# Performance work log

Hardware: AMD Instinct MI355X
Metric: run time of the kernel (lower is better)

## Reference

```python
import jax, jax.numpy as jnp
import numpy as np

V, E, H = 50000, 300, 256  # vocab, word dim, per-direction hidden (nfeat_sent=2H=512)
B, T = 256, 64
NEG = -1e9


def _lstm_scan(x, mask, w_ih, w_hh, b):
    """x: [T,B,E], mask: [T,B,1] float. Masked steps keep (h,c) unchanged.
    Gate order matches torch.nn.LSTM: i, f, g, o."""
    Bsz = x.shape[1]
    Hd = w_hh.shape[1]
    init = (jnp.zeros((Bsz, Hd), x.dtype), jnp.zeros((Bsz, Hd), x.dtype))

    def step(carry, inp):
        h, c = carry
        xt, mt = inp
        z = xt @ w_ih.T + h @ w_hh.T + b  # [B,4H]
        i, f, g, o = jnp.split(z, 4, axis=-1)
        i = jax.nn.sigmoid(i); f = jax.nn.sigmoid(f)
        g = jnp.tanh(g); o = jax.nn.sigmoid(o)
        c_new = f * c + i * g
        h_new = o * jnp.tanh(c_new)
        c = mt * c_new + (1.0 - mt) * c
        h = mt * h_new + (1.0 - mt) * h
        return (h, c), h

    _, hs = jax.lax.scan(step, init, (x, mask))
    return hs  # [T,B,H]


def setup_inputs() -> dict:
    key = jax.random.key(0)
    ks = jax.random.split(key, 9)
    token_ids = jax.random.randint(ks[0], (B, T), 0, V, dtype=jnp.int32)
    lengths = jax.random.randint(ks[1], (B,), 1, T + 1, dtype=jnp.int32)
    emb = jax.random.normal(ks[2], (V, E), jnp.float32) * 0.1
    s = 0.05
    w_ih_f = jax.random.normal(ks[3], (4 * H, E), jnp.float32) * s
    w_hh_f = jax.random.normal(ks[4], (4 * H, H), jnp.float32) * s
    b_f = jax.random.normal(ks[5], (4 * H,), jnp.float32) * s  # b_ih + b_hh fused
    w_ih_b = jax.random.normal(ks[6], (4 * H, E), jnp.float32) * s
    w_hh_b = jax.random.normal(ks[7], (4 * H, H), jnp.float32) * s
    b_b = jax.random.normal(ks[8], (4 * H,), jnp.float32) * s
    return {"token_ids": token_ids, "lengths": lengths, "emb": emb,
            "w_ih_f": w_ih_f, "w_hh_f": w_hh_f, "b_f": b_f,
            "w_ih_b": w_ih_b, "w_hh_b": w_hh_b, "b_b": b_b}


def reference(token_ids, lengths, emb, w_ih_f, w_hh_f, b_f, w_ih_b, w_hh_b, b_b):
    # Batched equivalent of the per-sentence loop: embed -> biLSTM -> max over time.
    x = emb[token_ids]                              # [B,T,E]
    x = jnp.swapaxes(x, 0, 1)                       # [T,B,E] (time-major)
    valid = (jnp.arange(T)[:, None] < lengths[None, :])  # [T,B]
    mask = valid.astype(x.dtype)[:, :, None]        # [T,B,1]

    h_fwd = _lstm_scan(x, mask, w_ih_f, w_hh_f, b_f)  # [T,B,H]
    # Backward direction: reverse time; masked (pad) steps leave state at zero,
    # so each sentence's backward pass starts exactly at its last real token.
    h_bwd = _lstm_scan(x[::-1], mask[::-1], w_ih_b, w_hh_b, b_b)[::-1]

    out = jnp.concatenate([h_fwd, h_bwd], axis=-1)  # [T,B,2H]
    out = jnp.where(valid[:, :, None], out, NEG)
    return jnp.max(out, axis=0)                     # [B, 2H] == [B, nfeat_sent]
```

## Files before the change

### kernel.cpp

```cpp
#include <hip/hip_runtime.h>
#include <hip/hip_bf16.h>
#include <math.h>

#define VV 50000
#define EE 300
#define HD 256
#define BB 256
#define TT 64
#define NEGV -1e9f

#define OFF_HF   0
#define OFF_CTR  524288
#define OFF_B2   526336
#define OFF_WHHF 528384
#define OFF_WIHF 1052672
#define WS_FULL_BYTES (1380352ULL * 4ULL)
#define FB_H 0
#define FB_C 262144

typedef __attribute__((ext_vector_type(8))) short bf16x8;
typedef __attribute__((ext_vector_type(4))) float f32x4;

__device__ __forceinline__ float sigf(float x) {
  return 1.f / (1.f + __expf(-x));
}
__device__ __forceinline__ float tanhfast(float x) {
  return 1.f - 2.f / (__expf(2.f * x) + 1.f);
}
__device__ __forceinline__ unsigned short f2bf(float f) {
  union { float f; unsigned u; } x;
  x.f = f;
  unsigned r = x.u + 0x7fffu + ((x.u >> 16) & 1u);
  return (unsigned short)(r >> 16);
}

__global__ __launch_bounds__(256) void prep_all(
    const float* __restrict__ whf, const float* __restrict__ whb,
    const float* __restrict__ wif, const float* __restrict__ wib,
    const float* __restrict__ bf, const float* __restrict__ bb,
    float* __restrict__ ws) {
  int idx = blockIdx.x * 256 + threadIdx.x;
  if (idx < 131072) ws[OFF_HF + idx] = 0.f;
  if (idx < 2048) {
    ((unsigned int*)(ws + OFF_CTR))[idx] = 0u;
    int dir = idx >> 10, jg = idx & 1023, j = jg >> 2, g = jg & 3;
    ws[OFF_B2 + idx] = (dir ? bb : bf)[g * HD + j];
  }
  if (idx < 65536) {
    int lane = idx & 63, kt = (idx >> 6) & 7, ngrp = (idx >> 9) & 63,
        dir = idx >> 15;
    int n = ngrp * 16 + (lane & 15);
    int j = n >> 2, g = n & 3;
    int k0 = kt * 32 + (lane >> 4) * 8;
    const float* W = dir ? whb : whf;
    const float* src = W + (size_t)((g << 8) + j) * HD + k0;
    union { unsigned short u[8]; uint4 q; } hp, lp;
#pragma unroll
    for (int e = 0; e < 8; ++e) {
      float v = src[e];
      unsigned short hh = f2bf(v);
      union { unsigned u; float f; } hf;
      hf.u = (unsigned)hh << 16;
      hp.u[e] = hh;
      lp.u[e] = f2bf(v - hf.f);
    }
    unsigned short* dst = (unsigned short*)(ws + OFF_WHHF) + (size_t)idx * 16;
    *(uint4*)dst = hp.q;
    *(uint4*)(dst + 8) = lp.q;
  }
  if (idx < 81920) {
    int lane = idx & 63;
    int f = idx >> 6;
    int kt = f % 10;
    int ngrp = (f / 10) & 63;
    int dir = f / 640;
    int n = ngrp * 16 + (lane & 15);
    int j = n >> 2, g = n & 3;
    int k0 = kt * 32 + (lane >> 4) * 8;
    const float* W = dir ? wib : wif;
    union { unsigned short u[8]; uint4 q; } p;
#pragma unroll
    for (int e = 0; e < 8; ++e) {
      int k = k0 + e;
      p.u[e] = (k < EE) ? f2bf(W[(size_t)((g << 8) + j) * EE + k])
                        : (unsigned short)0;
    }
    *(uint4*)((unsigned short*)(ws + OFF_WIHF) + (size_t)idx * 8) = p.q;
  }
}

__global__ __launch_bounds__(256) void init_kernel(float* __restrict__ ws,
                                                   float* __restrict__ out) {
  int idx = blockIdx.x * 256 + threadIdx.x;
  if (idx < 393216) ws[idx] = 0.f;
  if (idx < BB * 2 * HD) out[idx] = NEGV;
}

__global__ __launch_bounds__(512) void lstm_persist(
    const int* __restrict__ tok, const int* __restrict__ lens,
    const float* __restrict__ emb, float* __restrict__ ws,
    float* __restrict__ out) {
  const int bg = blockIdx.x;
  const int slice = blockIdx.y;
  const int dir = blockIdx.z;
  const int tid = threadIdx.x;
  const int lane = tid & 63;
  const int wv = tid >> 6;

  __shared__ __align__(16) unsigned short hfr[2][512][8];
  __shared__ __align__(16) unsigned short ebuf[2][5120];

  bf16x8 whi[8], wlo[8], wih[10];
  const int ngrp = slice * 8 + wv;
  {
    const unsigned short* p = (const unsigned short*)(ws + OFF_WHHF) +
                              (size_t)(((dir * 64 + ngrp) * 8) * 64 + lane) * 16;
#pragma unroll
    for (int kt = 0; kt < 8; ++kt) {
      whi[kt] = *(const bf16x8*)(p + kt * 1024);
      wlo[kt] = *(const bf16x8*)(p + kt * 1024 + 8);
    }
    const unsigned short* q = (const unsigned short*)(ws + OFF_WIHF) +
                              (size_t)(((dir * 64 + ngrp) * 10) * 64 + lane) * 8;
#pragma unroll
    for (int kt = 0; kt < 10; ++kt) wih[kt] = *(const bf16x8*)(q + kt * 512);
  }

  const int rg = tid >> 5;
  const int k8 = tid & 31;
  const int stage_row = bg * 16 + rg;
  const int strow = stage_row * TT;
  const int o2 = 32 + (k8 & 7);
  const bool has2 = (k8 < 8);
  const int slot1 = (k8 >> 2) * 64 + rg * 4 + (k8 & 3);
  const int slot2 = ((o2 >> 2) * 64) + rg * 4 + (o2 & 3);

  const int q = lane & 3;
  const int base = lane & 12;
  const int r = (lane >> 4) * 4 + q;
  const int gate_row = bg * 16 + r;
  const int len = lens[gate_row];
  const int jloc = ngrp * 4 + (base >> 2);
  const float4 bias4 =
      *(const float4*)(ws + OFF_B2 + dir * 1024 + ngrp * 16 + base);
  const int slot_j = (jloc >> 5) * 64 + r * 4 + ((jloc >> 3) & 3);
  const int e_j = jloc & 7;

  const int ld_slot = (lane & 15) * 4 + (lane >> 4);

  unsigned int* ctr =
      (unsigned int*)(ws + OFF_CTR) + (size_t)(dir * 16 + bg) * 32;
  unsigned short* hfg = (unsigned short*)(ws + OFF_HF);

  float c = 0.f, omax = NEGV, h_prev = 0.f;

  {
    const int t0 = dir ? (TT - 1) : 0;
    const float* er = emb + (size_t)tok[strow + t0] * EE;
    float4 a0 = *(const float4*)(er + k8 * 8);
    float4 a1 = *(const float4*)(er + k8 * 8 + 4);
    union { unsigned short u[8]; uint4 q; } p;
    p.u[0] = f2bf(a0.x); p.u[1] = f2bf(a0.y); p.u[2] = f2bf(a0.z);
    p.u[3] = f2bf(a0.w); p.u[4] = f2bf(a1.x); p.u[5] = f2bf(a1.y);
    p.u[6] = f2bf(a1.z); p.u[7] = f2bf(a1.w);
    *(uint4*)&ebuf[0][slot1 * 8] = p.q;
    if (has2) {
      float4 b0 = make_float4(0.f, 0.f, 0.f, 0.f);
      float4 b1 = make_float4(0.f, 0.f, 0.f, 0.f);
      if (o2 <= 37) b0 = *(const float4*)(er + o2 * 8);
      if (o2 < 37) b1 = *(const float4*)(er + o2 * 8 + 4);
      union { unsigned short u[8]; uint4 q; } p2;
      p2.u[0] = f2bf(b0.x); p2.u[1] = f2bf(b0.y); p2.u[2] = f2bf(b0.z);
      p2.u[3] = f2bf(b0.w); p2.u[4] = f2bf(b1.x); p2.u[5] = f2bf(b1.y);
      p2.u[6] = f2bf(b1.z); p2.u[7] = f2bf(b1.w);
      *(uint4*)&ebuf[0][slot2 * 8] = p2.q;
    }
  }

  for (int s = 0; s < TT; ++s) {
    const int t = dir ? (TT - 1 - s) : s;
    const bool nstage = (s < TT - 1);
    const unsigned long long* hsrc = (const unsigned long long*)(
        hfg + (size_t)(((s & 1) * 2 + dir) * 16 + bg) * 8192);
    unsigned long long hu0 = __hip_atomic_load(hsrc + tid * 4 + 0,
                                               __ATOMIC_RELAXED,
                                               __HIP_MEMORY_SCOPE_AGENT);
    unsigned long long hu1 = __hip_atomic_load(hsrc + tid * 4 + 1,
                                               __ATOMIC_RELAXED,
                                               __HIP_MEMORY_SCOPE_AGENT);
    unsigned long long hu2 = __hip_atomic_load(hsrc + tid * 4 + 2,
                                               __ATOMIC_RELAXED,
                                               __HIP_MEMORY_SCOPE_AGENT);
    unsigned long long hu3 = __hip_atomic_load(hsrc + tid * 4 + 3,
                                               __ATOMIC_RELAXED,
                                               __HIP_MEMORY_SCOPE_AGENT);
    float4 pe0, pe1, qe0, qe1;
    if (nstage) {
      const int tn = dir ? (TT - 2 - s) : (s + 1);
      const float* er = emb + (size_t)tok[strow + tn] * EE;
      pe0 = *(const float4*)(er + k8 * 8);
      pe1 = *(const float4*)(er + k8 * 8 + 4);
      qe0 = make_float4(0.f, 0.f, 0.f, 0.f);
      qe1 = make_float4(0.f, 0.f, 0.f, 0.f);
      if (has2) {
        if (o2 <= 37) qe0 = *(const float4*)(er + o2 * 8);
        if (o2 < 37) qe1 = *(const float4*)(er + o2 * 8 + 4);
      }
    }
    {
      unsigned long long* hdst_l = (unsigned long long*)hfr;
      hdst_l[tid * 4 + 0] = hu0;
      hdst_l[tid * 4 + 1] = hu1;
      hdst_l[tid * 4 + 2] = hu2;
      hdst_l[tid * 4 + 3] = hu3;
    }
    __syncthreads();
    f32x4 acc[4];
#pragma unroll
    for (int i = 0; i < 4; ++i) {
      acc[i][0] = 0.f; acc[i][1] = 0.f; acc[i][2] = 0.f; acc[i][3] = 0.f;
    }
    const unsigned short* eb = ebuf[s & 1];
#pragma unroll
    for (int kt = 0; kt < 10; ++kt) {
      bf16x8 ax = *(const bf16x8*)(eb + (kt * 64 + ld_slot) * 8);
      acc[kt & 3] =
          __builtin_amdgcn_mfma_f32_16x16x32_bf16(ax, wih[kt], acc[kt & 3], 0, 0, 0);
    }
#pragma unroll
    for (int kt = 0; kt < 8; ++kt) {
      bf16x8 ahi = *(const bf16x8*)&hfr[0][kt * 64 + ld_slot][0];
      bf16x8 alo = *(const bf16x8*)&hfr[1][kt * 64 + ld_slot][0];
      f32x4 a = acc[kt & 3];
      a = __builtin_amdgcn_mfma_f32_16x16x32_bf16(ahi, whi[kt], a, 0, 0, 0);
      a = __builtin_amdgcn_mfma_f32_16x16x32_bf16(alo, whi[kt], a, 0, 0, 0);
      a = __builtin_amdgcn_mfma_f32_16x16x32_bf16(ahi, wlo[kt], a, 0, 0, 0);
      acc[kt & 3] = a;
    }
    f32x4 zf = (acc[0] + acc[1]) + (acc[2] + acc[3]);
    float v0 = zf[0], v1 = zf[1], v2 = zf[2], v3 = zf[3];
    {
      float s0 = __shfl_xor(v1, 1), s1 = __shfl_xor(v0, 1);
      float s2 = __shfl_xor(v3, 1), s3 = __shfl_xor(v2, 1);
      const bool qb = (q & 1) != 0;
      float a0 = qb ? s0 : v0;
      float a1 = qb ? v1 : s1;
      float a2 = qb ? s2 : v2;
      float a3 = qb ? v3 : s3;
      float t0 = __shfl_xor(a2, 2), t1 = __shfl_xor(a3, 2);
      float t2 = __shfl_xor(a0, 2), t3 = __shfl_xor(a1, 2);
      const bool q2 = (q & 2) != 0;
      v0 = q2 ? t0 : a0;
      v1 = q2 ? t1 : a1;
      v2 = q2 ? a2 : t2;
      v3 = q2 ? a3 : t3;
    }
    float h_out = h_prev;
    if (t < len) {
      float ig = sigf(v0 + bias4.x);
      float fg = sigf(v1 + bias4.y);
      float gg = tanhfast(v2 + bias4.z);
      float og = sigf(v3 + bias4.w);
      c = fg * c + ig * gg;
      float hn = og * tanhfast(c);
      h_out = hn;
      omax = fmaxf(omax, hn);
    }
    h_prev = h_out;
    if (nstage) {
      unsigned short hi = f2bf(h_out);
      union { unsigned u; float f; } hf;
      hf.u = (unsigned)hi << 16;
      unsigned short lo = f2bf(h_out - hf.f);
      unsigned short* hdst =
          hfg + (size_t)((((s + 1) & 1) * 2 + dir) * 16 + bg) * 8192;
      __hip_atomic_store(hdst + slot_j * 8 + e_j, hi, __ATOMIC_RELAXED,
                         __HIP_MEMORY_SCOPE_AGENT);
      __hip_atomic_store(hdst + 4096 + slot_j * 8 + e_j, lo, __ATOMIC_RELAXED,
                         __HIP_MEMORY_SCOPE_AGENT);
      unsigned short* ebn = ebuf[(s + 1) & 1];
      {
        union { unsigned short u[8]; uint4 q; } p;
        p.u[0] = f2bf(pe0.x); p.u[1] = f2bf(pe0.y); p.u[2] = f2bf(pe0.z);
        p.u[3] = f2bf(pe0.w); p.u[4] = f2bf(pe1.x); p.u[5] = f2bf(pe1.y);
        p.u[6] = f2bf(pe1.z); p.u[7] = f2bf(pe1.w);
        *(uint4*)&ebn[slot1 * 8] = p.q;
        if (has2) {
          union { unsigned short u[8]; uint4 q; } p2;
          p2.u[0] = f2bf(qe0.x); p2.u[1] = f2bf(qe0.y); p2.u[2] = f2bf(qe0.z);
          p2.u[3] = f2bf(qe0.w); p2.u[4] = f2bf(qe1.x); p2.u[5] = f2bf(qe1.y);
          p2.u[6] = f2bf(qe1.z); p2.u[7] = f2bf(qe1.w);
          *(uint4*)&ebn[slot2 * 8] = p2.q;
        }
      }
      asm volatile("s_waitcnt vmcnt(0)" ::: "memory");
      __syncthreads();
      if (tid == 0) {
        __hip_atomic_fetch_add(ctr, 1u, __ATOMIC_RELAXED,
                               __HIP_MEMORY_SCOPE_AGENT);
      }
      if (tid < 64) {
        const unsigned int target = 8u * (unsigned)(s + 1);
        while (__hip_atomic_load(ctr, __ATOMIC_RELAXED,
                                 __HIP_MEMORY_SCOPE_AGENT) < target) {
        }
      }
      __syncthreads();
      asm volatile("" ::: "memory");
    }
  }
  out[(size_t)gate_row * (2 * HD) + dir * HD + jloc] = omax;
}

__global__ __launch_bounds__(256) void step_fused(
    const int* __restrict__ tok, const int* __restrict__ lens,
    const float* __restrict__ emb,
    const float* __restrict__ wih_f, const float* __restrict__ whh_f,
    const float* __restrict__ bias_f,
    const float* __restrict__ wih_b, const float* __restrict__ whh_b,
    const float* __restrict__ bias_b,
    float* __restrict__ ws, float* __restrict__ out, int s) {
  const int tid = threadIdx.x;
  const int jt = blockIdx.x, bt = blockIdx.y, dir = blockIdx.z;
  const int j0 = jt * 32, b0g = bt * 16;
  const int t = (dir == 0) ? s : (TT - 1 - s);
  const float* Wih = dir ? wih_b : wih_f;
  const float* Whh = dir ? whh_b : whh_f;
  const float* bias = dir ? bias_b : bias_f;
  const float* hcur = ws + FB_H + (size_t)((s & 1) * 2 + dir) * BB * HD;
  float* hnxt = ws + FB_H + (size_t)(((s + 1) & 1) * 2 + dir) * BB * HD;
  float* cbuf = ws + FB_C + (size_t)dir * BB * HD;

  __shared__ float a_sm[16][64];
  __shared__ float w_sm[64][132];
  __shared__ float z_sm[16][132];

  const int cg = tid & 31, bgr = tid >> 5;
  float acc[2][4] = {{0.f, 0.f, 0.f, 0.f}, {0.f, 0.f, 0.f, 0.f}};

  for (int phase = 0; phase < 2; ++phase) {
    const float* W = phase ? Whh : Wih;
    const int K = phase ? HD : EE;
    for (int k0 = 0; k0 < K; k0 += 64) {
      const int klen = (K - k0) < 64 ? (K - k0) : 64;
      {
        int bl = tid >> 4, kk4 = tid & 15;
        if (kk4 * 4 < klen) {
          const float* src;
          if (phase == 0) {
            int tk = tok[(b0g + bl) * TT + t];
            src = emb + (size_t)tk * EE + k0 + kk4 * 4;
          } else {
            src = hcur + (size_t)(b0g + bl) * HD + k0 + kk4 * 4;
          }
          *(float4*)&a_sm[bl][kk4 * 4] = *(const float4*)src;
        }
      }
      for (int i = 0; i < 8; ++i) {
        int e = i * 256 + tid;
        int col = e >> 4, kk4 = e & 15;
        if (kk4 * 4 < klen) {
          int gcol = ((col >> 5) * HD) + j0 + (col & 31);
          float4 v = *(const float4*)(W + (size_t)gcol * K + k0 + kk4 * 4);
          w_sm[kk4 * 4 + 0][col] = v.x;
          w_sm[kk4 * 4 + 1][col] = v.y;
          w_sm[kk4 * 4 + 2][col] = v.z;
          w_sm[kk4 * 4 + 3][col] = v.w;
        }
      }
      __syncthreads();
      for (int k = 0; k < klen; ++k) {
        float a0 = a_sm[bgr * 2 + 0][k];
        float a1 = a_sm[bgr * 2 + 1][k];
        float4 w = *(const float4*)&w_sm[k][cg * 4];
        acc[0][0] += a0 * w.x; acc[0][1] += a0 * w.y;
        acc[0][2] += a0 * w.z; acc[0][3] += a0 * w.w;
        acc[1][0] += a1 * w.x; acc[1][1] += a1 * w.y;
        acc[1][2] += a1 * w.z; acc[1][3] += a1 * w.w;
      }
      __syncthreads();
    }
  }
  *(float4*)&z_sm[bgr * 2 + 0][cg * 4] =
      make_float4(acc[0][0], acc[0][1], acc[0][2], acc[0][3]);
  *(float4*)&z_sm[bgr * 2 + 1][cg * 4] =
      make_float4(acc[1][0], acc[1][1], acc[1][2], acc[1][3]);
  __syncthreads();
  for (int pi = 0; pi < 2; ++pi) {
    int p = pi * 256 + tid;
    int bl = p >> 5, jl = p & 31;
    int bglob = b0g + bl, jglob = j0 + jl;
    bool valid = t < lens[bglob];
    float h_old = hcur[(size_t)bglob * HD + jglob];
    float h_out = h_old;
    if (valid) {
      float zi = z_sm[bl][0 + jl] + bias[0 * HD + jglob];
      float zf = z_sm[bl][32 + jl] + bias[1 * HD + jglob];
      float zg = z_sm[bl][64 + jl] + bias[2 * HD + jglob];
      float zo = z_sm[bl][96 + jl] + bias[3 * HD + jglob];
      float ig = sigf(zi), fg = sigf(zf), gg = tanhf(zg), og = sigf(zo);
      float c_old = cbuf[(size_t)bglob * HD + jglob];
      float c_new = fg * c_old + ig * gg;
      float h_new = og * tanhf(c_new);
      cbuf[(size_t)bglob * HD + jglob] = c_new;
      h_out = h_new;
      float* op = out + (size_t)bglob * (2 * HD) + dir * HD + jglob;
      *op = fmaxf(*op, h_new);
    }
    hnxt[(size_t)bglob * HD + jglob] = h_out;
  }
}

extern "C" void kernel_launch(void* const* d_in, const int* in_sizes, int n_in,
                              void* d_out, int out_size, void* d_ws,
                              size_t ws_size, hipStream_t stream) {
  const int* tok = (const int*)d_in[0];
  const int* lens = (const int*)d_in[1];
  const float* emb = (const float*)d_in[2];
  const float* wih_f = (const float*)d_in[3];
  const float* whh_f = (const float*)d_in[4];
  const float* b_f = (const float*)d_in[5];
  const float* wih_b = (const float*)d_in[6];
  const float* whh_b = (const float*)d_in[7];
  const float* b_b = (const float*)d_in[8];
  float* out = (float*)d_out;
  float* ws = (float*)d_ws;

  const bool full = ws_size >= WS_FULL_BYTES;
  if (full) {
    hipLaunchKernelGGL(prep_all, dim3(512), dim3(256), 0, stream, whh_f,
                       whh_b, wih_f, wih_b, b_f, b_b, ws);
    hipLaunchKernelGGL(lstm_persist, dim3(16, 8, 2), dim3(512), 0, stream,
                       tok, lens, emb, ws, out);
  } else {
    hipLaunchKernelGGL(init_kernel, dim3(1536), dim3(256), 0, stream, ws, out);
    for (int s = 0; s < TT; ++s) {
      hipLaunchKernelGGL(step_fused, dim3(8, 16, 2), dim3(256), 0, stream, tok,
                         lens, emb, wih_f, whh_f, b_f, wih_b, whh_b, b_b, ws,
                         out, s);
    }
  }
}
```

Baseline: 229.1 us.

## Coalesce recurrent h exchange through LDS staging and swizzle LDS slots

Each block now stages its new hidden-state values (bf16 hi/lo pairs) in a shared-memory tile and has 128 threads write them to global memory as packed 64-bit atomic stores. Before, every thread issued two scattered 16-bit atomic stores. The LDS slot layout for embeddings and h fragments is XOR-swizzled to reduce bank conflicts on the MFMA operand reads, and the global h load pattern is changed to match. This adds an extra __syncthreads and an LDS round trip per time step on the critical recurrent path, in exchange for far fewer global store transactions before the cross-block barrier.

```diff
diff --git a/kernel.cpp b/kernel.cpp
--- a/kernel.cpp
+++ b/kernel.cpp
@@ -109,6 +109,7 @@
 
   __shared__ __align__(16) unsigned short hfr[2][512][8];
   __shared__ __align__(16) unsigned short ebuf[2][5120];
+  __shared__ unsigned int hx[16][36];
 
   bf16x8 whi[8], wlo[8], wih[10];
   const int ngrp = slice * 8 + wv;
@@ -132,8 +133,9 @@
   const int strow = stage_row * TT;
   const int o2 = 32 + (k8 & 7);
   const bool has2 = (k8 < 8);
-  const int slot1 = (k8 >> 2) * 64 + rg * 4 + (k8 & 3);
-  const int slot2 = ((o2 >> 2) * 64) + rg * 4 + (o2 & 3);
+  const int swz_r = (rg >> 1) & 3;
+  const int slot1 = (k8 >> 2) * 64 + rg * 4 + ((k8 & 3) ^ swz_r);
+  const int slot2 = (o2 >> 2) * 64 + rg * 4 + ((o2 & 3) ^ swz_r);
 
   const int q = lane & 3;
   const int base = lane & 12;
@@ -141,12 +143,12 @@
   const int gate_row = bg * 16 + r;
   const int len = lens[gate_row];
   const int jloc = ngrp * 4 + (base >> 2);
+  const int jl32 = wv * 4 + (base >> 2);
   const float4 bias4 =
       *(const float4*)(ws + OFF_B2 + dir * 1024 + ngrp * 16 + base);
-  const int slot_j = (jloc >> 5) * 64 + r * 4 + ((jloc >> 3) & 3);
-  const int e_j = jloc & 7;
-
-  const int ld_slot = (lane & 15) * 4 + (lane >> 4);
+
+  const int ld_r = lane & 15, ld_oct = lane >> 4;
+  const int ld_slot = ld_r * 4 + (ld_oct ^ ((ld_r >> 1) & 3));
 
   unsigned int* ctr =
       (unsigned int*)(ws + OFF_CTR) + (size_t)(dir * 16 + bg) * 32;
@@ -182,18 +184,18 @@
     const bool nstage = (s < TT - 1);
     const unsigned long long* hsrc = (const unsigned long long*)(
         hfg + (size_t)(((s & 1) * 2 + dir) * 16 + bg) * 8192);
-    unsigned long long hu0 = __hip_atomic_load(hsrc + tid * 4 + 0,
-                                               __ATOMIC_RELAXED,
-                                               __HIP_MEMORY_SCOPE_AGENT);
-    unsigned long long hu1 = __hip_atomic_load(hsrc + tid * 4 + 1,
-                                               __ATOMIC_RELAXED,
-                                               __HIP_MEMORY_SCOPE_AGENT);
-    unsigned long long hu2 = __hip_atomic_load(hsrc + tid * 4 + 2,
-                                               __ATOMIC_RELAXED,
-                                               __HIP_MEMORY_SCOPE_AGENT);
-    unsigned long long hu3 = __hip_atomic_load(hsrc + tid * 4 + 3,
-                                               __ATOMIC_RELAXED,
-                                               __HIP_MEMORY_SCOPE_AGENT);
+    unsigned long long a0 = __hip_atomic_load(hsrc + 2 * tid + 0,
+                                              __ATOMIC_RELAXED,
+                                              __HIP_MEMORY_SCOPE_AGENT);
+    unsigned long long a1 = __hip_atomic_load(hsrc + 2 * tid + 1,
+                                              __ATOMIC_RELAXED,
+                                              __HIP_MEMORY_SCOPE_AGENT);
+    unsigned long long b0 = __hip_atomic_load(hsrc + 1024 + 2 * tid + 0,
+                                              __ATOMIC_RELAXED,
+                                              __HIP_MEMORY_SCOPE_AGENT);
+    unsigned long long b1 = __hip_atomic_load(hsrc + 1024 + 2 * tid + 1,
+                                              __ATOMIC_RELAXED,
+                                              __HIP_MEMORY_SCOPE_AGENT);
     float4 pe0, pe1, qe0, qe1;
     if (nstage) {
       const int tn = dir ? (TT - 2 - s) : (s + 1);
@@ -208,11 +210,14 @@
       }
     }
     {
-      unsigned long long* hdst_l = (unsigned long long*)hfr;
-      hdst_l[tid * 4 + 0] = hu0;
-      hdst_l[tid * 4 + 1] = hu1;
-      hdst_l[tid * 4 + 2] = hu2;
-      hdst_l[tid * 4 + 3] = hu3;
+      unsigned long long* l0 =
+          (unsigned long long*)((char*)&hfr[0][0][0] + tid * 16);
+      l0[0] = a0;
+      l0[1] = a1;
+      unsigned long long* l1 =
+          (unsigned long long*)((char*)&hfr[0][0][0] + 8192 + tid * 16);
+      l1[0] = b0;
+      l1[1] = b1;
     }
     __syncthreads();
     f32x4 acc[4];
@@ -243,17 +248,17 @@
       float s0 = __shfl_xor(v1, 1), s1 = __shfl_xor(v0, 1);
       float s2 = __shfl_xor(v3, 1), s3 = __shfl_xor(v2, 1);
       const bool qb = (q & 1) != 0;
-      float a0 = qb ? s0 : v0;
-      float a1 = qb ? v1 : s1;
-      float a2 = qb ? s2 : v2;
-      float a3 = qb ? v3 : s3;
-      float t0 = __shfl_xor(a2, 2), t1 = __shfl_xor(a3, 2);
-      float t2 = __shfl_xor(a0, 2), t3 = __shfl_xor(a1, 2);
+      float t0a = qb ? s0 : v0;
+      float t1a = qb ? v1 : s1;
+      float t2a = qb ? s2 : v2;
+      float t3a = qb ? v3 : s3;
+      float u0 = __shfl_xor(t2a, 2), u1 = __shfl_xor(t3a, 2);
+      float u2 = __shfl_xor(t0a, 2), u3 = __shfl_xor(t1a, 2);
       const bool q2 = (q & 2) != 0;
-      v0 = q2 ? t0 : a0;
-      v1 = q2 ? t1 : a1;
-      v2 = q2 ? a2 : t2;
-      v3 = q2 ? a3 : t3;
+      v0 = q2 ? u0 : t0a;
+      v1 = q2 ? u1 : t1a;
+      v2 = q2 ? t2a : u2;
+      v3 = q2 ? t3a : u3;
     }
     float h_out = h_prev;
     if (t < len) {
@@ -268,16 +273,13 @@
     }
     h_prev = h_out;
     if (nstage) {
-      unsigned short hi = f2bf(h_out);
-      union { unsigned u; float f; } hf;
-      hf.u = (unsigned)hi << 16;
-      unsigned short lo = f2bf(h_out - hf.f);
-      unsigned short* hdst =
-          hfg + (size_t)((((s + 1) & 1) * 2 + dir) * 16 + bg) * 8192;
-      __hip_atomic_store(hdst + slot_j * 8 + e_j, hi, __ATOMIC_RELAXED,
-                         __HIP_MEMORY_SCOPE_AGENT);
-      __hip_atomic_store(hdst + 4096 + slot_j * 8 + e_j, lo, __ATOMIC_RELAXED,
-                         __HIP_MEMORY_SCOPE_AGENT);
+      {
+        unsigned short hi = f2bf(h_out);
+        union { unsigned u; float f; } hf;
+        hf.u = (unsigned)hi << 16;
+        unsigned short lo = f2bf(h_out - hf.f);
+        hx[r][jl32] = ((unsigned)hi << 16) | (unsigned)lo;
+      }
       unsigned short* ebn = ebuf[(s + 1) & 1];
       {
         union { unsigned short u[8]; uint4 q; } p;
@@ -292,6 +294,42 @@
           p2.u[6] = f2bf(qe1.z); p2.u[7] = f2bf(qe1.w);
           *(uint4*)&ebn[slot2 * 8] = p2.q;
         }
+      }
+      __syncthreads();
+      if (tid < 128) {
+        const int part = tid >> 6;
+        const int sl = tid & 63;
+        const int wr = sl >> 2;
+        const int woct = (sl & 3) ^ ((wr >> 1) & 3);
+        uint4 w0 = *(const uint4*)&hx[wr][woct * 8];
+        uint4 w1 = *(const uint4*)&hx[wr][woct * 8 + 4];
+        unsigned long long q0, q1;
+        if (part == 0) {
+          q0 = ((unsigned long long)(w0.x >> 16)) |
+               ((unsigned long long)(w0.y >> 16) << 16) |
+               ((unsigned long long)(w0.z >> 16) << 32) |
+               ((unsigned long long)(w0.w >> 16) << 48);
+          q1 = ((unsigned long long)(w1.x >> 16)) |
+               ((unsigned long long)(w1.y >> 16) << 16) |
+               ((unsigned long long)(w1.z >> 16) << 32) |
+               ((unsigned long long)(w1.w >> 16) << 48);
+        } else {
+          q0 = ((unsigned long long)(w0.x & 0xffffu)) |
+               ((unsigned long long)(w0.y & 0xffffu) << 16) |
+               ((unsigned long long)(w0.z & 0xffffu) << 32) |
+               ((unsigned long long)(w0.w & 0xffffu) << 48);
+          q1 = ((unsigned long long)(w1.x & 0xffffu)) |
+               ((unsigned long long)(w1.y & 0xffffu) << 16) |
+               ((unsigned long long)(w1.z & 0xffffu) << 32) |
+               ((unsigned long long)(w1.w & 0xffffu) << 48);
+        }
+        unsigned long long* hdst = (unsigned long long*)(
+            hfg + (size_t)((((s + 1) & 1) * 2 + dir) * 16 + bg) * 8192 +
+            part * 4096 + (slice * 64 + sl) * 8);
+        __hip_atomic_store(hdst + 0, q0, __ATOMIC_RELAXED,
+                           __HIP_MEMORY_SCOPE_AGENT);
+        __hip_atomic_store(hdst + 1, q1, __ATOMIC_RELAXED,
+                           __HIP_MEMORY_SCOPE_AGENT);
       }
       asm volatile("s_waitcnt vmcnt(0)" ::: "memory");
       __syncthreads();
```

New measurement: 218.7 us. 4.5% less time.
